# Optimization experiments

Hardware: AMD Instinct MI355X
Metric: run time of the kernel (lower is better)

## Reference

```python
import jax, jax.numpy as jnp
import numpy as np

NUM_HEADS = 8
EPS = 1e-9


def setup_inputs() -> dict:
    key = jax.random.key(0)
    ks = jax.random.split(key, 8)
    B, N, D = 2, 2048, 512
    s = 1.0 / np.sqrt(D)
    x = jax.random.normal(ks[0], (B, N, D), dtype=jnp.float32)
    adjacency = jax.random.uniform(ks[1], (B, N, N), dtype=jnp.float32)
    # Linear weights stored as (in, out) so application is x @ W + b
    W_q = jax.random.normal(ks[2], (D, D), dtype=jnp.float32) * s
    W_k = jax.random.normal(ks[3], (D, D), dtype=jnp.float32) * s
    W_v = jax.random.normal(ks[4], (D, D), dtype=jnp.float32) * s
    b_q = jnp.zeros((D,), jnp.float32)
    b_k = jnp.zeros((D,), jnp.float32)
    b_v = jnp.zeros((D,), jnp.float32)
    # soul_gate: Linear(2D -> 1); weight stored as flat (2D,), bias scalar
    w_g = jax.random.normal(ks[5], (2 * D,), dtype=jnp.float32) * (1.0 / np.sqrt(2 * D))
    b_g = jnp.zeros((), jnp.float32)
    return {"x": x, "adjacency": adjacency, "W_q": W_q, "b_q": b_q,
            "W_k": W_k, "b_k": b_k, "W_v": W_v, "b_v": b_v,
            "w_g": w_g, "b_g": b_g}


def reference(x, adjacency, W_q, b_q, W_k, b_k, W_v, b_v, w_g, b_g):
    B, N, D = x.shape
    H = NUM_HEADS
    hd = D // H
    Q = (x @ W_q + b_q).reshape(B, N, H, hd)
    K = (x @ W_k + b_k).reshape(B, N, H, hd)
    V = (x @ W_v + b_v).reshape(B, N, H, hd)
    scores = jnp.einsum('bihd,bjhd->bhij', Q, K) / jnp.sqrt(jnp.float32(hd))
    # soul_gate(cat[x_i, x_j]) is linear, so it decomposes exactly:
    # bias[b,i,j] = x[b,i]@w_g[:D] + x[b,j]@w_g[D:] + b_g  (same math, no (B,N,N,2D) tensor)
    a = x @ w_g[:D]          # (B, N) contribution of x_i
    c = x @ w_g[D:]          # (B, N) contribution of x_j
    soul_bias = a[:, :, None] + c[:, None, :] + b_g   # (B, N, N)
    scores = scores + (soul_bias + jnp.log(adjacency + EPS))[:, None, :, :]
    attn = jax.nn.softmax(scores, axis=-1)            # (B, H, N, N)
    out = jnp.einsum('bhij,bjhd->bihd', attn, V).reshape(B, N, D)
    return out + x
```

## Files before the change

### kernel.cpp

```cpp
#include <hip/hip_runtime.h>
#include <hip/hip_bf16.h>

typedef __bf16 bf16x8 __attribute__((ext_vector_type(8)));
typedef float f32x4 __attribute__((ext_vector_type(4)));
typedef unsigned short u16x8 __attribute__((ext_vector_type(8)));

#define LOG2E 1.44269504f

__device__ __forceinline__ unsigned short f2bu(float f) {
    __hip_bfloat16 h = __float2bfloat16(f);
    unsigned short u;
    __builtin_memcpy(&u, &h, 2);
    return u;
}

__device__ __forceinline__ float fexp2(float x) {
#if __has_builtin(__builtin_amdgcn_exp2f)
    return __builtin_amdgcn_exp2f(x);
#else
    return __expf(x * 0.69314718f);
#endif
}

__device__ __forceinline__ float bu2f(unsigned short u) {
    unsigned int v = ((unsigned int)u) << 16;
    float f;
    __builtin_memcpy(&f, &v, 4);
    return f;
}

#define GLDS16(gp, lp) __builtin_amdgcn_global_load_lds( \
    (const __attribute__((address_space(1))) unsigned int*)(gp), \
    (__attribute__((address_space(3))) unsigned int*)(lp), 16, 0, 0)

#define OFF_QS  0u
#define OFF_KB  4194304u
#define OFF_VT  8388608u
#define OFF_CV  12582912u
#define OFF_XB  12599296u
#define OFF_WT  16793600u
#define OFF_MQ  18366464u
#define OFF_PO  35143680u
#define OFF_PL  51920896u

__global__ void k_prepwt(const float* __restrict__ x, const float* __restrict__ wg,
                         const float* __restrict__ w0, const float* __restrict__ w1,
                         const float* __restrict__ w2,
                         unsigned short* __restrict__ xb, float* __restrict__ cv2,
                         unsigned short* __restrict__ wt) {
    if (blockIdx.x < 1024) {
        int row = blockIdx.x * 4 + (threadIdx.x >> 6);
        int l = threadIdx.x & 63;
        const float4* xr = reinterpret_cast<const float4*>(x + (size_t)row * 512);
        float4 a = xr[l * 2], b2 = xr[l * 2 + 1];
        ushort4 o0, o1;
        o0.x = f2bu(a.x);  o0.y = f2bu(a.y);  o0.z = f2bu(a.z);  o0.w = f2bu(a.w);
        o1.x = f2bu(b2.x); o1.y = f2bu(b2.y); o1.z = f2bu(b2.z); o1.w = f2bu(b2.w);
        ushort4* dst = reinterpret_cast<ushort4*>(xb + (size_t)row * 512);
        dst[l * 2] = o0; dst[l * 2 + 1] = o1;
        const float4* wr = reinterpret_cast<const float4*>(wg + 512);
        float4 g0 = wr[l * 2], g1 = wr[l * 2 + 1];
        float s = a.x * g0.x + a.y * g0.y + a.z * g0.z + a.w * g0.w
                + b2.x * g1.x + b2.y * g1.y + b2.z * g1.z + b2.w * g1.w;
#pragma unroll
        for (int off = 32; off >= 1; off >>= 1) s += __shfl_xor(s, off, 64);
        if (l == 0) cv2[row] = fexp2((s - 8.0f) * LOG2E);
    } else {
        int bid2 = blockIdx.x - 1024;
        int z = bid2 >> 6, yy = bid2 & 63;
        int k0 = (yy >> 3) * 64, n0 = (yy & 7) * 64;
        const float* W = (z == 0) ? w0 : ((z == 1) ? w1 : w2);
        __shared__ float T[64][65];
        int c = threadIdx.x & 63, r0 = threadIdx.x >> 6;
#pragma unroll
        for (int i = 0; i < 16; i++) { int r = r0 + i * 4; T[r][c] = W[(k0 + r) * 512 + n0 + c]; }
        __syncthreads();
        unsigned short* Wt = wt + z * (512 * 512);
#pragma unroll
        for (int i = 0; i < 16; i++) { int a = r0 + i * 4; Wt[(n0 + a) * 512 + k0 + c] = f2bu(T[c][a]); }
    }
}

__global__ __launch_bounds__(256) void k_mid(
    const float* __restrict__ adj, const float* __restrict__ cv2,
    unsigned short* __restrict__ mq,
    const unsigned short* __restrict__ xb, const unsigned short* __restrict__ wt,
    const float* __restrict__ bq, const float* __restrict__ bk, const float* __restrict__ bv,
    unsigned short* __restrict__ Qs, unsigned short* __restrict__ Kb,
    unsigned short* __restrict__ Vt) {
    if (blockIdx.x >= 384) {
        int blk = blockIdx.x - 384;
        int bic = blk >> 4, jtp = blk & 15;
        int b = bic >> 7, ic = bic & 127;
        int t = threadIdx.x;
        int l = t >> 2, mt = t & 3, q = l >> 4, cl = l & 15;
        const float* arow = adj + ((size_t)(b * 2048 + ic * 16 + cl)) * 2048;
        const float* cvb = cv2 + b * 2048;
#pragma unroll
        for (int e = 0; e < 2; e++) {
            int jt = jtp * 2 + e;
            int j0 = jt * 64 + 16 * mt + q * 4;
            const float4 av = *reinterpret_cast<const float4*>(arow + j0);
            const float4 cv = *reinterpret_cast<const float4*>(cvb + j0);
            ushort4 o;
            o.x = f2bu((av.x + 1e-9f) * cv.x);
            o.y = f2bu((av.y + 1e-9f) * cv.y);
            o.z = f2bu((av.z + 1e-9f) * cv.z);
            o.w = f2bu((av.w + 1e-9f) * cv.w);
            *reinterpret_cast<ushort4*>(mq + (size_t)bic * 32768 + jt * 1024 + l * 16 + mt * 4) = o;
        }
        return;
    }
    int gid = blockIdx.x;
    int bx = gid & 31, by = (gid >> 5) & 3, z = gid >> 7;
    __shared__ __align__(16) unsigned short As[128 * 32];
    __shared__ __align__(16) unsigned short Bs[128 * 32];
    const unsigned short* Wt = wt + z * (512 * 512);
    const float* bias = (z == 0) ? bq : ((z == 1) ? bk : bv);
    float scale = (z == 0) ? (0.125f * LOG2E) : 1.0f;
    int m0 = bx * 128, n0 = by * 128;
    int tid = threadIdx.x, w = tid >> 6, l = tid & 63;
    int q = l >> 4, cl = l & 15;
    int wr = w >> 1, wc = w & 1;
    f32x4 acc[4][4];
#pragma unroll
    for (int mi = 0; mi < 4; mi++)
#pragma unroll
        for (int ni = 0; ni < 4; ni++)
#pragma unroll
            for (int r = 0; r < 4; r++) acc[mi][ni][r] = 0.f;
    int arow = l >> 2, ach = (l & 3) * 8;
    for (int k0 = 0; k0 < 512; k0 += 32) {
#pragma unroll
        for (int e = 0; e < 2; e++) {
            GLDS16(xb + (size_t)(m0 + w * 32 + e * 16 + arow) * 512 + k0 + ach, As + (w * 32 + e * 16) * 32);
            GLDS16(Wt + (size_t)(n0 + w * 32 + e * 16 + arow) * 512 + k0 + ach, Bs + (w * 32 + e * 16) * 32);
        }
        __syncthreads();
        bf16x8 af[4], bfr[4];
#pragma unroll
        for (int i = 0; i < 4; i++) {
            af[i]  = *reinterpret_cast<const bf16x8*>(As + (wr * 64 + i * 16 + cl) * 32 + q * 8);
            bfr[i] = *reinterpret_cast<const bf16x8*>(Bs + (wc * 64 + i * 16 + cl) * 32 + q * 8);
        }
#pragma unroll
        for (int mi = 0; mi < 4; mi++)
#pragma unroll
            for (int ni = 0; ni < 4; ni++)
                acc[mi][ni] = __builtin_amdgcn_mfma_f32_16x16x32_bf16(af[mi], bfr[ni], acc[mi][ni], 0, 0, 0);
        __syncthreads();
    }
    if (z == 2) {
        int b_ = (m0 + wr * 64) >> 11;
#pragma unroll
        for (int mi = 0; mi < 4; mi++) {
            int n_ = (m0 + wr * 64 + mi * 16 + q * 4) & 2047;
#pragma unroll
            for (int ni = 0; ni < 4; ni++) {
                int col = n0 + wc * 64 + ni * 16 + cl;
                int h_ = col >> 6, d_ = col & 63;
                float bv_ = bias[col];
                ushort4 o;
                o.x = f2bu(acc[mi][ni][0] + bv_); o.y = f2bu(acc[mi][ni][1] + bv_);
                o.z = f2bu(acc[mi][ni][2] + bv_); o.w = f2bu(acc[mi][ni][3] + bv_);
                *reinterpret_cast<ushort4*>(Vt + ((size_t)((b_ * 8 + h_) * 64 + d_)) * 2048 + n_) = o;
            }
        }
    } else {
        unsigned short* Cout = (z == 0) ? Qs : Kb;
#pragma unroll
        for (int mi = 0; mi < 4; mi++)
#pragma unroll
            for (int ni = 0; ni < 4; ni++) {
                int col = n0 + wc * 64 + ni * 16 + cl;
                float bv_ = bias[col];
#pragma unroll
                for (int r = 0; r < 4; r++) {
                    int row = m0 + wr * 64 + mi * 16 + q * 4 + r;
                    Cout[(size_t)row * 512 + col] = f2bu((acc[mi][ni][r] + bv_) * scale);
                }
            }
    }
}

__global__ __launch_bounds__(256, 3) void k_attn(
    const unsigned short* __restrict__ Qs, const unsigned short* __restrict__ Kb,
    const unsigned short* __restrict__ Vt, const unsigned short* __restrict__ mq,
    unsigned short* __restrict__ PO, float* __restrict__ PL) {
    __shared__ __align__(16) unsigned short Ks[2][4096];
    __shared__ __align__(16) unsigned short Vs[2][4096];
    __shared__ __align__(16) unsigned short PA[4][32 * 72];
    int bid = blockIdx.x;
    int h = bid >> 7, b = (bid >> 6) & 1, ig = (bid >> 2) & 15, js = bid & 3;
    int tid = threadIdx.x, w = tid >> 6, l = tid & 63, q = l >> 4, cl = l & 15;
    int bh = b * 8 + h;
    int ic0 = ig * 8 + w * 2;

    bf16x8 qf[2][2];
#pragma unroll
    for (int rc = 0; rc < 2; rc++) {
        const unsigned short* qp = Qs + (size_t)(b * 2048 + ig * 128 + w * 32 + rc * 16 + cl) * 512 + h * 64 + q * 8;
        qf[rc][0] = *reinterpret_cast<const bf16x8*>(qp);
        qf[rc][1] = *reinterpret_cast<const bf16x8*>(qp + 32);
    }
    bf16x8 ones;
#pragma unroll
    for (int i = 0; i < 8; i++) { unsigned short o1 = 0x3F80; __builtin_memcpy(((unsigned short*)&ones) + i, &o1, 2); }

    f32x4 O[2][4];
    f32x4 Osum[2];
#pragma unroll
    for (int rc = 0; rc < 2; rc++) {
#pragma unroll
        for (int nt = 0; nt < 4; nt++)
#pragma unroll
            for (int r = 0; r < 4; r++) O[rc][nt][r] = 0.f;
#pragma unroll
        for (int r = 0; r < 4; r++) Osum[rc][r] = 0.f;
    }

    const unsigned short* Kh = Kb + (size_t)b * 2048 * 512 + h * 64;
    const unsigned short* Vh = Vt + ((size_t)bh * 64) * 2048;
    const unsigned short* mb0 = mq + (size_t)(b * 128 + ic0) * 32768 + l * 16 + (size_t)(js * 8) * 1024;
    const unsigned short* mb1 = mb0 + 32768;
    unsigned short* pw = &PA[w][0];
    int lrow = l >> 2, lch = (l & 3) * 8;
    int jb0 = js * 512;

#pragma unroll
    for (int e = 0; e < 2; e++) {
        int c = w * 2 + e, kk = c >> 2, r16 = (c & 3) * 16;
        GLDS16(Kh + (size_t)(jb0 + r16 + lrow) * 512 + kk * 32 + lch, &Ks[0][kk * 2048 + r16 * 32]);
        GLDS16(Vh + (size_t)(r16 + lrow) * 2048 + jb0 + kk * 32 + lch, &Vs[0][kk * 2048 + r16 * 32]);
    }
    u16x8 mcA[2][2], mcB[2][2];
    mcA[0][0] = *reinterpret_cast<const u16x8*>(mb0);
    mcA[0][1] = *reinterpret_cast<const u16x8*>(mb0 + 8);
    mcA[1][0] = *reinterpret_cast<const u16x8*>(mb1);
    mcA[1][1] = *reinterpret_cast<const u16x8*>(mb1 + 8);

#define ATT_BODY(T, BUF, MCC, MCN, PRED) { \
    __syncthreads();    \
    if (PRED) { \
        int jb = jb0 + ((T) + 1) * 64; \
        _Pragma("unroll") \
        for (int e = 0; e < 2; e++) { \
            int c = w * 2 + e, kk = c >> 2, r16 = (c & 3) * 16; \
            GLDS16(Kh + (size_t)(jb + r16 + lrow) * 512 + kk * 32 + lch, &Ks[(BUF) ^ 1][kk * 2048 + r16 * 32]); \
            GLDS16(Vh + (size_t)(r16 + lrow) * 2048 + jb + kk * 32 + lch, &Vs[(BUF) ^ 1][kk * 2048 + r16 * 32]); \
        } \
        size_t off = (size_t)((T) + 1) * 1024; \
        MCN[0][0] = *reinterpret_cast<const u16x8*>(mb0 + off); \
        MCN[0][1] = *reinterpret_cast<const u16x8*>(mb0 + off + 8); \
        MCN[1][0] = *reinterpret_cast<const u16x8*>(mb1 + off); \
        MCN[1][1] = *reinterpret_cast<const u16x8*>(mb1 + off + 8); \
    } \
     \
    f32x4 S[2][4]; \
    _Pragma("unroll") \
    for (int rc = 0; rc < 2; rc++) \
        _Pragma("unroll") \
        for (int mt = 0; mt < 4; mt++) \
            _Pragma("unroll") \
            for (int r = 0; r < 4; r++) S[rc][mt][r] = 0.f; \
    __builtin_amdgcn_s_setprio(1); \
    _Pragma("unroll") \
    for (int mt = 0; mt < 4; mt++) { \
        bf16x8 kf0 = *reinterpret_cast<const bf16x8*>(&Ks[BUF][(16 * mt + cl) * 32 + q * 8]); \
        bf16x8 kf1 = *reinterpret_cast<const bf16x8*>(&Ks[BUF][2048 + (16 * mt + cl) * 32 + q * 8]); \
        _Pragma("unroll") \
        for (int rc = 0; rc < 2; rc++) { \
            S[rc][mt] = __builtin_amdgcn_mfma_f32_16x16x32_bf16(kf0, qf[rc][0], S[rc][mt], 0, 0, 0); \
            S[rc][mt] = __builtin_amdgcn_mfma_f32_16x16x32_bf16(kf1, qf[rc][1], S[rc][mt], 0, 0, 0); \
        } \
    } \
    __builtin_amdgcn_s_setprio(0); \
     \
    _Pragma("unroll") \
    for (int rc = 0; rc < 2; rc++) { \
        _Pragma("unroll") \
        for (int mt = 0; mt < 4; mt++) { \
            float p0 = fexp2(S[rc][mt][0]) * bu2f((mt < 2) ? MCC[rc][0][mt * 4 + 0] : MCC[rc][1][(mt - 2) * 4 + 0]); \
            float p1 = fexp2(S[rc][mt][1]) * bu2f((mt < 2) ? MCC[rc][0][mt * 4 + 1] : MCC[rc][1][(mt - 2) * 4 + 1]); \
            float p2 = fexp2(S[rc][mt][2]) * bu2f((mt < 2) ? MCC[rc][0][mt * 4 + 2] : MCC[rc][1][(mt - 2) * 4 + 2]); \
            float p3 = fexp2(S[rc][mt][3]) * bu2f((mt < 2) ? MCC[rc][0][mt * 4 + 3] : MCC[rc][1][(mt - 2) * 4 + 3]); \
            ushort4 o; \
            o.x = f2bu(p0); o.y = f2bu(p1); o.z = f2bu(p2); o.w = f2bu(p3); \
            *reinterpret_cast<ushort4*>(pw + rc * (16 * 72) + cl * 72 + 16 * mt + q * 4) = o; \
        } \
    } \
     \
    __builtin_amdgcn_s_setprio(1); \
    _Pragma("unroll") \
    for (int jc = 0; jc < 2; jc++) { \
        bf16x8 pf0 = *reinterpret_cast<const bf16x8*>(pw + cl * 72 + jc * 32 + q * 8); \
        bf16x8 pf1 = *reinterpret_cast<const bf16x8*>(pw + 16 * 72 + cl * 72 + jc * 32 + q * 8); \
        _Pragma("unroll") \
        for (int nt = 0; nt < 4; nt++) { \
            bf16x8 vf = *reinterpret_cast<const bf16x8*>(&Vs[BUF][jc * 2048 + (16 * nt + cl) * 32 + q * 8]); \
            O[0][nt] = __builtin_amdgcn_mfma_f32_16x16x32_bf16(pf0, vf, O[0][nt], 0, 0, 0); \
            O[1][nt] = __builtin_amdgcn_mfma_f32_16x16x32_bf16(pf1, vf, O[1][nt], 0, 0, 0); \
        } \
        Osum[0] = __builtin_amdgcn_mfma_f32_16x16x32_bf16(pf0, ones, Osum[0], 0, 0, 0); \
        Osum[1] = __builtin_amdgcn_mfma_f32_16x16x32_bf16(pf1, ones, Osum[1], 0, 0, 0); \
    } \
    __builtin_amdgcn_s_setprio(0); \
}

    for (int tt = 0; tt < 4; tt++) {
        int t0 = tt * 2;
        ATT_BODY(t0, 0, mcA, mcB, 1)
        ATT_BODY(t0 + 1, 1, mcB, mcA, (tt < 3))
    }
#undef ATT_BODY

    typedef unsigned short u16x8s __attribute__((ext_vector_type(8)));
#pragma unroll
    for (int rc = 0; rc < 2; rc++) {
        size_t chunk = ((size_t)(bh * 128 + ic0 + rc)) * 4 + js;
        unsigned short* po = PO + chunk * 1024 + l * 16;
        u16x8s o01, o23;
#pragma unroll
        for (int nt = 0; nt < 4; nt++) {
            o01[nt]     = f2bu(O[rc][nt][0]);
            o01[4 + nt] = f2bu(O[rc][nt][1]);
            o23[nt]     = f2bu(O[rc][nt][2]);
            o23[4 + nt] = f2bu(O[rc][nt][3]);
        }
        *reinterpret_cast<u16x8s*>(po) = o01;
        *reinterpret_cast<u16x8s*>(po + 8) = o23;
        if (cl == 0) {
#pragma unroll
            for (int r = 0; r < 4; r++)
                PL[chunk * 16 + q * 4 + r] = Osum[rc][r];
        }
    }
}

__global__ void k_comb(const unsigned short* __restrict__ PO, const float* __restrict__ PL,
                       const float* __restrict__ x, float* __restrict__ out) {
    int blk = blockIdx.x;
    int t64 = blk & 31, bh = blk >> 5;
    int b = bh >> 3, h = bh & 7;
    int t = threadIdx.x;
    int l = t >> 2, r = t & 3, q = l >> 4, cl = l & 15;
#pragma unroll
    for (int w = 0; w < 4; w++) {
        int ic = t64 * 4 + w;
        size_t c0 = ((size_t)(bh * 128 + ic)) * 4;
        float o0 = 0.f, o1 = 0.f, o2 = 0.f, o3 = 0.f, lsum = 0.f;
#pragma unroll
        for (int js = 0; js < 4; js++) {
            ushort4 a = *reinterpret_cast<const ushort4*>(PO + (c0 + js) * 1024 + t * 4);
            o0 += bu2f(a.x); o1 += bu2f(a.y); o2 += bu2f(a.z); o3 += bu2f(a.w);
            lsum += PL[(c0 + js) * 16 + q * 4 + r];
        }
        float inv = 1.0f / lsum;
        size_t gro = (size_t)(b * 2048 + ic * 16 + q * 4 + r) * 512 + h * 64;
        out[gro + 0 * 16 + cl] = o0 * inv + x[gro + 0 * 16 + cl];
        out[gro + 1 * 16 + cl] = o1 * inv + x[gro + 1 * 16 + cl];
        out[gro + 2 * 16 + cl] = o2 * inv + x[gro + 2 * 16 + cl];
        out[gro + 3 * 16 + cl] = o3 * inv + x[gro + 3 * 16 + cl];
    }
}

extern "C" void kernel_launch(void* const* d_in, const int* in_sizes, int n_in,
                              void* d_out, int out_size, void* d_ws, size_t ws_size,
                              hipStream_t stream) {
    const float* x   = (const float*)d_in[0];
    const float* adj = (const float*)d_in[1];
    const float* Wq  = (const float*)d_in[2];
    const float* bq  = (const float*)d_in[3];
    const float* Wk  = (const float*)d_in[4];
    const float* bk  = (const float*)d_in[5];
    const float* Wv  = (const float*)d_in[6];
    const float* bv  = (const float*)d_in[7];
    const float* wg  = (const float*)d_in[8];
    float* out = (float*)d_out;
    char* ws = (char*)d_ws;
    unsigned short* Qs = (unsigned short*)(ws + OFF_QS);
    unsigned short* Kb = (unsigned short*)(ws + OFF_KB);
    unsigned short* Vt = (unsigned short*)(ws + OFF_VT);
    float* cv2 = (float*)(ws + OFF_CV);
    unsigned short* xb = (unsigned short*)(ws + OFF_XB);
    unsigned short* wt = (unsigned short*)(ws + OFF_WT);
    unsigned short* mqp = (unsigned short*)(ws + OFF_MQ);
    unsigned short* PO = (unsigned short*)(ws + OFF_PO);
    float* PL = (float*)(ws + OFF_PL);

    k_prepwt<<<1216, 256, 0, stream>>>(x, wg, Wq, Wk, Wv, xb, cv2, wt);
    k_mid<<<4480, 256, 0, stream>>>(adj, cv2, mqp, xb, wt, bq, bk, bv, Qs, Kb, Vt);
    k_attn<<<1024, 256, 0, stream>>>(Qs, Kb, Vt, mqp, PO, PL);
    k_comb<<<512, 256, 0, stream>>>(PO, PL, x, out);
}
```

Measured before the change: 149.8 us.

## Load V fragments directly to registers and compute row sums with VALU

```diff
diff --git a/kernel.cpp b/kernel.cpp
--- a/kernel.cpp
+++ b/kernel.cpp
@@ -188,7 +188,6 @@
     const unsigned short* __restrict__ Vt, const unsigned short* __restrict__ mq,
     unsigned short* __restrict__ PO, float* __restrict__ PL) {
     __shared__ __align__(16) unsigned short Ks[2][4096];
-    __shared__ __align__(16) unsigned short Vs[2][4096];
     __shared__ __align__(16) unsigned short PA[4][32 * 72];
     int bid = blockIdx.x;
     int h = bid >> 7, b = (bid >> 6) & 1, ig = (bid >> 2) & 15, js = bid & 3;
@@ -203,21 +202,15 @@
         qf[rc][0] = *reinterpret_cast<const bf16x8*>(qp);
         qf[rc][1] = *reinterpret_cast<const bf16x8*>(qp + 32);
     }
-    bf16x8 ones;
-#pragma unroll
-    for (int i = 0; i < 8; i++) { unsigned short o1 = 0x3F80; __builtin_memcpy(((unsigned short*)&ones) + i, &o1, 2); }
 
     f32x4 O[2][4];
-    f32x4 Osum[2];
-#pragma unroll
-    for (int rc = 0; rc < 2; rc++) {
+#pragma unroll
+    for (int rc = 0; rc < 2; rc++)
 #pragma unroll
         for (int nt = 0; nt < 4; nt++)
 #pragma unroll
             for (int r = 0; r < 4; r++) O[rc][nt][r] = 0.f;
-#pragma unroll
-        for (int r = 0; r < 4; r++) Osum[rc][r] = 0.f;
-    }
+    float ls[2] = {0.f, 0.f};
 
     const unsigned short* Kh = Kb + (size_t)b * 2048 * 512 + h * 64;
     const unsigned short* Vh = Vt + ((size_t)bh * 64) * 2048;
@@ -226,12 +219,12 @@
     unsigned short* pw = &PA[w][0];
     int lrow = l >> 2, lch = (l & 3) * 8;
     int jb0 = js * 512;
+    const unsigned short* Vl = Vh + (size_t)cl * 2048 + jb0 + q * 8;
 
 #pragma unroll
     for (int e = 0; e < 2; e++) {
         int c = w * 2 + e, kk = c >> 2, r16 = (c & 3) * 16;
         GLDS16(Kh + (size_t)(jb0 + r16 + lrow) * 512 + kk * 32 + lch, &Ks[0][kk * 2048 + r16 * 32]);
-        GLDS16(Vh + (size_t)(r16 + lrow) * 2048 + jb0 + kk * 32 + lch, &Vs[0][kk * 2048 + r16 * 32]);
     }
     u16x8 mcA[2][2], mcB[2][2];
     mcA[0][0] = *reinterpret_cast<const u16x8*>(mb0);
@@ -241,13 +234,20 @@
 
 #define ATT_BODY(T, BUF, MCC, MCN, PRED) { \
     __syncthreads();    \
+     \
+    bf16x8 vfr[2][4]; \
+    _Pragma("unroll") \
+    for (int jc = 0; jc < 2; jc++) \
+        _Pragma("unroll") \
+        for (int nt = 0; nt < 4; nt++) \
+            vfr[jc][nt] = *reinterpret_cast<const bf16x8*>(Vl + (size_t)(nt * 16) * 2048 + (T) * 64 + jc * 32); \
+    __builtin_amdgcn_sched_barrier(0); \
     if (PRED) { \
         int jb = jb0 + ((T) + 1) * 64; \
         _Pragma("unroll") \
         for (int e = 0; e < 2; e++) { \
             int c = w * 2 + e, kk = c >> 2, r16 = (c & 3) * 16; \
             GLDS16(Kh + (size_t)(jb + r16 + lrow) * 512 + kk * 32 + lch, &Ks[(BUF) ^ 1][kk * 2048 + r16 * 32]); \
-            GLDS16(Vh + (size_t)(r16 + lrow) * 2048 + jb + kk * 32 + lch, &Vs[(BUF) ^ 1][kk * 2048 + r16 * 32]); \
         } \
         size_t off = (size_t)((T) + 1) * 1024; \
         MCN[0][0] = *reinterpret_cast<const u16x8*>(mb0 + off); \
@@ -286,6 +286,7 @@
             float p3 = fexp2(S[rc][mt][3]) * bu2f((mt < 2) ? MCC[rc][0][mt * 4 + 3] : MCC[rc][1][(mt - 2) * 4 + 3]); \
             ushort4 o; \
             o.x = f2bu(p0); o.y = f2bu(p1); o.z = f2bu(p2); o.w = f2bu(p3); \
+            ls[rc] += (bu2f(o.x) + bu2f(o.y)) + (bu2f(o.z) + bu2f(o.w)); \
             *reinterpret_cast<ushort4*>(pw + rc * (16 * 72) + cl * 72 + 16 * mt + q * 4) = o; \
         } \
     } \
@@ -297,12 +298,9 @@
         bf16x8 pf1 = *reinterpret_cast<const bf16x8*>(pw + 16 * 72 + cl * 72 + jc * 32 + q * 8); \
         _Pragma("unroll") \
         for (int nt = 0; nt < 4; nt++) { \
-            bf16x8 vf = *reinterpret_cast<const bf16x8*>(&Vs[BUF][jc * 2048 + (16 * nt + cl) * 32 + q * 8]); \
-            O[0][nt] = __builtin_amdgcn_mfma_f32_16x16x32_bf16(pf0, vf, O[0][nt], 0, 0, 0); \
-            O[1][nt] = __builtin_amdgcn_mfma_f32_16x16x32_bf16(pf1, vf, O[1][nt], 0, 0, 0); \
+            O[0][nt] = __builtin_amdgcn_mfma_f32_16x16x32_bf16(pf0, vfr[jc][nt], O[0][nt], 0, 0, 0); \
+            O[1][nt] = __builtin_amdgcn_mfma_f32_16x16x32_bf16(pf1, vfr[jc][nt], O[1][nt], 0, 0, 0); \
         } \
-        Osum[0] = __builtin_amdgcn_mfma_f32_16x16x32_bf16(pf0, ones, Osum[0], 0, 0, 0); \
-        Osum[1] = __builtin_amdgcn_mfma_f32_16x16x32_bf16(pf1, ones, Osum[1], 0, 0, 0); \
     } \
     __builtin_amdgcn_s_setprio(0); \
 }
@@ -329,11 +327,10 @@
         }
         *reinterpret_cast<u16x8s*>(po) = o01;
         *reinterpret_cast<u16x8s*>(po + 8) = o23;
-        if (cl == 0) {
-#pragma unroll
-            for (int r = 0; r < 4; r++)
-                PL[chunk * 16 + q * 4 + r] = Osum[rc][r];
-        }
+        float lsum = ls[rc];
+        lsum += __shfl_xor(lsum, 16, 64);
+        lsum += __shfl_xor(lsum, 32, 64);
+        if (q == 0) PL[chunk * 16 + cl] = lsum;
     }
 }
 
```

Measured after the change: 194.5 us. 29.9% more time.
